# Kernel tuning notes

Hardware: AMD Instinct MI355X
Metric: run time of the kernel (lower is better)

Reference implementation:

```python
import jax, jax.numpy as jnp
import numpy as np
import math

NEG_INF = -1e30  # stand-in for float('-inf'); softmax/logsumexp treat it identically


def _fnoise(x):
    # factorized NoisyNet transform f(x) = sign(x) * sqrt(|x|)
    return jnp.sign(x) * jnp.sqrt(jnp.abs(x))


def setup_inputs() -> dict:
    B, T, D, E = 4, 4096, 2048, 16
    key = jax.random.key(0)
    ks = jax.random.split(key, 6)
    sigma_init = 0.4 / math.sqrt(D)  # sigma_zero / sqrt(in_features)
    return {
        "mh_output": jax.random.normal(ks[0], (B, T, D), dtype=jnp.float32),
        "weight": jax.random.normal(ks[1], (E, D), dtype=jnp.float32) * 0.02,
        "sigma_weight": jnp.full((E, D), sigma_init, dtype=jnp.float32),
        "bias": jax.random.normal(ks[2], (E,), dtype=jnp.float32) * 0.02,
        "sigma_bias": jnp.full((E,), sigma_init, dtype=jnp.float32),
        "eps_in": jax.random.normal(ks[3], (D,), dtype=jnp.float32),
        "eps_out": jax.random.normal(ks[4], (E,), dtype=jnp.float32),
    }


def reference(mh_output, weight, sigma_weight, bias, sigma_bias, eps_in, eps_out):
    top_k = 2
    E = weight.shape[0]

    # NoisyFactorizedLinear: W' = W + sigma_W * (f(eps_out) f(eps_in)^T)
    f_in = _fnoise(eps_in)            # [D]
    f_out = _fnoise(eps_out)          # [E]
    w_noisy = weight + sigma_weight * (f_out[:, None] * f_in[None, :])  # [E, D]
    b_noisy = bias + sigma_bias * f_out                                 # [E]
    logits = jnp.einsum("btd,ed->bte", mh_output, w_noisy) + b_noisy    # [B,T,E]
    # dropout(p=0.125) is identity in eval mode

    top_vals, indices = jax.lax.top_k(logits, top_k)                    # [B,T,k]
    # scatter top-k back into a -inf-filled tensor == mask of selected experts
    keep = jnp.sum(jax.nn.one_hot(indices, E, dtype=jnp.bool_), axis=-2)  # [B,T,E]
    sparse_logits = jnp.where(keep, logits, NEG_INF)

    router_output = jax.nn.softmax(sparse_logits, axis=-1)

    # z-loss: mean(logsumexp(sparse_logits, -1)^2); only top-k entries survive
    lse = jax.scipy.special.logsumexp(top_vals, axis=-1)                # [B,T]
    z_loss = jnp.mean(lse ** 2)

    return router_output, indices, z_loss
```

## Files before the change

kernel.cpp:

```cpp
#include <hip/hip_runtime.h>
#include <math.h>

#define NROWS 16384
#define DDIM  2048
#define NEXP  16
#define RBLOCKS 1024
#define WPB 4
#define ZN (RBLOCKS * WPB)

__device__ __forceinline__ float fnoise(float x) {
    return copysignf(sqrtf(fabsf(x)), x);
}

__device__ __forceinline__ void async_copy16(const float4* g, float4* l) {
    __builtin_amdgcn_global_load_lds(
        (const __attribute__((address_space(1))) void*)g,
        (__attribute__((address_space(3))) void*)l, 16, 0, 0);
}


__global__ void prep_kernel(const float* __restrict__ weight,
                            const float* __restrict__ sigma_weight,
                            const float* __restrict__ bias,
                            const float* __restrict__ sigma_bias,
                            const float* __restrict__ eps_in,
                            const float* __restrict__ eps_out,
                            float* __restrict__ w_noisy,
                            float* __restrict__ b_noisy) {
    int gid = blockIdx.x * blockDim.x + threadIdx.x;
    int e  = gid >> 9;
    int c4 = gid & 511;
    float4 w  = ((const float4*)weight)[gid];
    float4 sw = ((const float4*)sigma_weight)[gid];
    float4 ei = ((const float4*)eps_in)[c4];
    float fo = fnoise(eps_out[e]);
    float4 r;
    r.x = w.x + sw.x * fo * fnoise(ei.x);
    r.y = w.y + sw.y * fo * fnoise(ei.y);
    r.z = w.z + sw.z * fo * fnoise(ei.z);
    r.w = w.w + sw.w * fo * fnoise(ei.w);
    ((float4*)w_noisy)[gid] = r;
    if (gid < 4) {
        float4 b  = ((const float4*)bias)[gid];
        float4 sb = ((const float4*)sigma_bias)[gid];
        float4 eo = ((const float4*)eps_out)[gid];
        float4 rb;
        rb.x = b.x + sb.x * fnoise(eo.x);
        rb.y = b.y + sb.y * fnoise(eo.y);
        rb.z = b.z + sb.z * fnoise(eo.z);
        rb.w = b.w + sb.w * fnoise(eo.w);
        ((float4*)b_noisy)[gid] = rb;
    }
}

__global__ __launch_bounds__(256, 4) void router_kernel(
        const float* __restrict__ x,
        const float* __restrict__ w_noisy,
        const float* __restrict__ b_noisy,
        float* __restrict__ out_router,
        float* __restrict__ out_idx,
        float* __restrict__ zpart) {
    __shared__ float4 wlds[2][NEXP * 64];

    const int tid  = threadIdx.x;
    const int wv   = tid >> 6;
    const int lane = tid & 63;

    const int rowBase = blockIdx.x * 16 + wv * 4;
    const float4* xr0 = (const float4*)(x + (size_t)(rowBase + 0) * DDIM);
    const float4* xr1 = (const float4*)(x + (size_t)(rowBase + 1) * DDIM);
    const float4* xr2 = (const float4*)(x + (size_t)(rowBase + 2) * DDIM);
    const float4* xr3 = (const float4*)(x + (size_t)(rowBase + 3) * DDIM);
    const float4* wsrc = (const float4*)w_noisy;

    float acc[64];
    #pragma unroll
    for (int i = 0; i < 64; ++i) acc[i] = 0.0f;

    float4 xbuf[2][4];

    #pragma unroll
    for (int j = 0; j < 4; ++j) {
        int fb = j * 256 + wv * 64;
        async_copy16(wsrc + (size_t)(fb >> 6) * 512 + lane, &wlds[0][fb]);
    }
    xbuf[0][0] = xr0[lane];
    xbuf[0][1] = xr1[lane];
    xbuf[0][2] = xr2[lane];
    xbuf[0][3] = xr3[lane];
    __syncthreads();

    #pragma unroll
    for (int c = 0; c < 8; ++c) {
        const int cb = c & 1;
        const int nb = cb ^ 1;
        const int xc = c & 1;
        const int xn = xc ^ 1;
        if (c < 7) {
            #pragma unroll
            for (int j = 0; j < 4; ++j) {
                int fb = j * 256 + wv * 64;
                async_copy16(wsrc + (size_t)(fb >> 6) * 512 + (c + 1) * 64 + lane,
                             &wlds[nb][fb]);
            }
            int p = (c + 1) * 64 + lane;
            xbuf[xn][0] = xr0[p];
            xbuf[xn][1] = xr1[p];
            xbuf[xn][2] = xr2[p];
            xbuf[xn][3] = xr3[p];
        }
        #pragma unroll
        for (int e = 0; e < 16; ++e) {
            float4 w = wlds[cb][e * 64 + lane];
            float s0 = acc[0 * 16 + e];
            float s1 = acc[1 * 16 + e];
            float s2 = acc[2 * 16 + e];
            float s3 = acc[3 * 16 + e];
            s0 = fmaf(xbuf[xc][0].x, w.x, s0); s0 = fmaf(xbuf[xc][0].y, w.y, s0);
            s0 = fmaf(xbuf[xc][0].z, w.z, s0); s0 = fmaf(xbuf[xc][0].w, w.w, s0);
            s1 = fmaf(xbuf[xc][1].x, w.x, s1); s1 = fmaf(xbuf[xc][1].y, w.y, s1);
            s1 = fmaf(xbuf[xc][1].z, w.z, s1); s1 = fmaf(xbuf[xc][1].w, w.w, s1);
            s2 = fmaf(xbuf[xc][2].x, w.x, s2); s2 = fmaf(xbuf[xc][2].y, w.y, s2);
            s2 = fmaf(xbuf[xc][2].z, w.z, s2); s2 = fmaf(xbuf[xc][2].w, w.w, s2);
            s3 = fmaf(xbuf[xc][3].x, w.x, s3); s3 = fmaf(xbuf[xc][3].y, w.y, s3);
            s3 = fmaf(xbuf[xc][3].z, w.z, s3); s3 = fmaf(xbuf[xc][3].w, w.w, s3);
            acc[0 * 16 + e] = s0;
            acc[1 * 16 + e] = s1;
            acc[2 * 16 + e] = s2;
            acc[3 * 16 + e] = s3;
        }
        if (c < 7) __syncthreads();
    }

    #pragma unroll
    for (int half = 32; half >= 1; half >>= 1) {
        #pragma unroll
        for (int i = 0; i < half; ++i) {
            bool hi = (lane & half) != 0;
            float keep = hi ? acc[i + half] : acc[i];
            float send = hi ? acc[i] : acc[i + half];
            float recv = __shfl_xor(send, half, 64);
            acc[i] = keep + recv;
        }
    }

    const int e = lane & 15;
    const int r = lane >> 4;
    const int row = rowBase + r;
    float logit = acc[0] + b_noisy[e];

    float m1 = logit; int i1 = e;
    #pragma unroll
    for (int off = 8; off >= 1; off >>= 1) {
        float om = __shfl_xor(m1, off, 64);
        int   oi = __shfl_xor(i1, off, 64);
        if (om > m1 || (om == m1 && oi < i1)) { m1 = om; i1 = oi; }
    }
    float v2 = (e == i1) ? -3.4e38f : logit;
    float m2 = v2; int i2 = e;
    #pragma unroll
    for (int off = 8; off >= 1; off >>= 1) {
        float om = __shfl_xor(m2, off, 64);
        int   oi = __shfl_xor(i2, off, 64);
        if (om > m2 || (om == m2 && oi < i2)) { m2 = om; i2 = oi; }
    }

    float t = expf(m2 - m1);
    float p1 = 1.0f / (1.0f + t);
    float val = (e == i1) ? p1 : ((e == i2) ? t * p1 : 0.0f);
    out_router[(size_t)rowBase * NEXP + lane] = val;

    if (e < 2) {
        out_idx[(size_t)row * 2 + e] = (float)((e == 0) ? i1 : i2);
    }

    float zv = 0.0f;
    if (e == 0) {
        float lse = m1 + log1pf(t);
        zv = lse * lse;
    }
    zv += __shfl_xor(zv, 16, 64);
    zv += __shfl_xor(zv, 32, 64);
    if (lane == 0) {
        zpart[blockIdx.x * WPB + wv] = zv;
    }
}

__global__ void finalize_kernel(const float* __restrict__ zpart,
                                float* __restrict__ out) {
    __shared__ float ws4[4];
    int tid = threadIdx.x;
    float s = 0.0f;
    for (int i = tid; i < ZN; i += 256) s += zpart[i];
    #pragma unroll
    for (int off = 32; off >= 1; off >>= 1) s += __shfl_xor(s, off, 64);
    if ((tid & 63) == 0) ws4[tid >> 6] = s;
    __syncthreads();
    if (tid == 0) {
        float total = ws4[0] + ws4[1] + ws4[2] + ws4[3];
        out[NROWS * NEXP + NROWS * 2] = total * (1.0f / (float)NROWS);
    }
}

extern "C" void kernel_launch(void* const* d_in, const int* in_sizes, int n_in,
                              void* d_out, int out_size, void* d_ws, size_t ws_size,
                              hipStream_t stream) {
    const float* mh      = (const float*)d_in[0];
    const float* weight  = (const float*)d_in[1];
    const float* sigw    = (const float*)d_in[2];
    const float* bias    = (const float*)d_in[3];
    const float* sigb    = (const float*)d_in[4];
    const float* eps_in  = (const float*)d_in[5];
    const float* eps_out = (const float*)d_in[6];

    float* out      = (float*)d_out;
    float* w_noisy  = (float*)d_ws;
    float* b_noisy  = w_noisy + NEXP * DDIM;
    float* zpart    = w_noisy + 32800;

    prep_kernel<<<32, 256, 0, stream>>>(
        weight, sigw, bias, sigb, eps_in, eps_out, w_noisy, b_noisy);

    router_kernel<<<RBLOCKS, 256, 0, stream>>>(
        mh, w_noisy, b_noisy, out, out + NROWS * NEXP, zpart);

    finalize_kernel<<<1, 256, 0, stream>>>(zpart, out);
}
```

Baseline: 211.2 us.

## Fuse noisy weight construction into router kernel, drop prep kernel

Removes the separate prep kernel and builds the noisy weight tile on the fly inside the router kernel. Each block loads weight, sigma and eps_in through registers, applies the factorized noise and writes the result into LDS, replacing the async global-to-LDS copy. The bias noise is also computed inline. This saves one kernel launch and its dependency, but every block now does twice the weight loads plus the noise arithmetic. It also holds more registers across the compute loop, which can hurt occupancy.

```diff
diff --git a/kernel.cpp b/kernel.cpp
--- a/kernel.cpp
+++ b/kernel.cpp
@@ -12,51 +12,15 @@
     return copysignf(sqrtf(fabsf(x)), x);
 }
 
-__device__ __forceinline__ void async_copy16(const float4* g, float4* l) {
-    __builtin_amdgcn_global_load_lds(
-        (const __attribute__((address_space(1))) void*)g,
-        (__attribute__((address_space(3))) void*)l, 16, 0, 0);
-}
-
-
-__global__ void prep_kernel(const float* __restrict__ weight,
-                            const float* __restrict__ sigma_weight,
-                            const float* __restrict__ bias,
-                            const float* __restrict__ sigma_bias,
-                            const float* __restrict__ eps_in,
-                            const float* __restrict__ eps_out,
-                            float* __restrict__ w_noisy,
-                            float* __restrict__ b_noisy) {
-    int gid = blockIdx.x * blockDim.x + threadIdx.x;
-    int e  = gid >> 9;
-    int c4 = gid & 511;
-    float4 w  = ((const float4*)weight)[gid];
-    float4 sw = ((const float4*)sigma_weight)[gid];
-    float4 ei = ((const float4*)eps_in)[c4];
-    float fo = fnoise(eps_out[e]);
-    float4 r;
-    r.x = w.x + sw.x * fo * fnoise(ei.x);
-    r.y = w.y + sw.y * fo * fnoise(ei.y);
-    r.z = w.z + sw.z * fo * fnoise(ei.z);
-    r.w = w.w + sw.w * fo * fnoise(ei.w);
-    ((float4*)w_noisy)[gid] = r;
-    if (gid < 4) {
-        float4 b  = ((const float4*)bias)[gid];
-        float4 sb = ((const float4*)sigma_bias)[gid];
-        float4 eo = ((const float4*)eps_out)[gid];
-        float4 rb;
-        rb.x = b.x + sb.x * fnoise(eo.x);
-        rb.y = b.y + sb.y * fnoise(eo.y);
-        rb.z = b.z + sb.z * fnoise(eo.z);
-        rb.w = b.w + sb.w * fnoise(eo.w);
-        ((float4*)b_noisy)[gid] = rb;
-    }
-}
 
 __global__ __launch_bounds__(256, 4) void router_kernel(
         const float* __restrict__ x,
-        const float* __restrict__ w_noisy,
-        const float* __restrict__ b_noisy,
+        const float* __restrict__ weight,
+        const float* __restrict__ sigma_w,
+        const float* __restrict__ bias,
+        const float* __restrict__ sigma_b,
+        const float* __restrict__ eps_in,
+        const float* __restrict__ eps_out,
         float* __restrict__ out_router,
         float* __restrict__ out_idx,
         float* __restrict__ zpart) {
@@ -71,7 +35,14 @@
     const float4* xr1 = (const float4*)(x + (size_t)(rowBase + 1) * DDIM);
     const float4* xr2 = (const float4*)(x + (size_t)(rowBase + 2) * DDIM);
     const float4* xr3 = (const float4*)(x + (size_t)(rowBase + 3) * DDIM);
-    const float4* wsrc = (const float4*)w_noisy;
+    const float4* wsrc = (const float4*)weight;
+    const float4* ssrc = (const float4*)sigma_w;
+    const float4* eisrc = (const float4*)eps_in;
+
+    float fo0 = fnoise(eps_out[0 * 4 + wv]);
+    float fo1 = fnoise(eps_out[1 * 4 + wv]);
+    float fo2 = fnoise(eps_out[2 * 4 + wv]);
+    float fo3 = fnoise(eps_out[3 * 4 + wv]);
 
     float acc[64];
     #pragma unroll
@@ -79,10 +50,23 @@
 
     float4 xbuf[2][4];
 
-    #pragma unroll
-    for (int j = 0; j < 4; ++j) {
-        int fb = j * 256 + wv * 64;
-        async_copy16(wsrc + (size_t)(fb >> 6) * 512 + lane, &wlds[0][fb]);
+    {
+        float4 ei = eisrc[lane];
+        float fi_x = fnoise(ei.x), fi_y = fnoise(ei.y);
+        float fi_z = fnoise(ei.z), fi_w = fnoise(ei.w);
+        #pragma unroll
+        for (int j = 0; j < 4; ++j) {
+            const float foj = (j == 0) ? fo0 : (j == 1) ? fo1 : (j == 2) ? fo2 : fo3;
+            size_t g = (size_t)(j * 4 + wv) * 512 + lane;
+            float4 w4 = wsrc[g];
+            float4 s4 = ssrc[g];
+            float4 r;
+            r.x = w4.x + s4.x * foj * fi_x;
+            r.y = w4.y + s4.y * foj * fi_y;
+            r.z = w4.z + s4.z * foj * fi_z;
+            r.w = w4.w + s4.w * foj * fi_w;
+            wlds[0][j * 256 + wv * 64 + lane] = r;
+        }
     }
     xbuf[0][0] = xr0[lane];
     xbuf[0][1] = xr1[lane];
@@ -96,13 +80,18 @@
         const int nb = cb ^ 1;
         const int xc = c & 1;
         const int xn = xc ^ 1;
+        float4 w40, w41, w42, w43, s40, s41, s42, s43, ei;
         if (c < 7) {
-            #pragma unroll
-            for (int j = 0; j < 4; ++j) {
-                int fb = j * 256 + wv * 64;
-                async_copy16(wsrc + (size_t)(fb >> 6) * 512 + (c + 1) * 64 + lane,
-                             &wlds[nb][fb]);
-            }
+            size_t col = (size_t)(c + 1) * 64 + lane;
+            ei  = eisrc[col];
+            w40 = wsrc[(size_t)(0 * 4 + wv) * 512 + col];
+            s40 = ssrc[(size_t)(0 * 4 + wv) * 512 + col];
+            w41 = wsrc[(size_t)(1 * 4 + wv) * 512 + col];
+            s41 = ssrc[(size_t)(1 * 4 + wv) * 512 + col];
+            w42 = wsrc[(size_t)(2 * 4 + wv) * 512 + col];
+            s42 = ssrc[(size_t)(2 * 4 + wv) * 512 + col];
+            w43 = wsrc[(size_t)(3 * 4 + wv) * 512 + col];
+            s43 = ssrc[(size_t)(3 * 4 + wv) * 512 + col];
             int p = (c + 1) * 64 + lane;
             xbuf[xn][0] = xr0[p];
             xbuf[xn][1] = xr1[p];
@@ -129,7 +118,24 @@
             acc[2 * 16 + e] = s2;
             acc[3 * 16 + e] = s3;
         }
-        if (c < 7) __syncthreads();
+        if (c < 7) {
+            float fi_x = fnoise(ei.x), fi_y = fnoise(ei.y);
+            float fi_z = fnoise(ei.z), fi_w = fnoise(ei.w);
+            float4 r;
+            r.x = w40.x + s40.x * fo0 * fi_x;  r.y = w40.y + s40.y * fo0 * fi_y;
+            r.z = w40.z + s40.z * fo0 * fi_z;  r.w = w40.w + s40.w * fo0 * fi_w;
+            wlds[nb][0 * 256 + wv * 64 + lane] = r;
+            r.x = w41.x + s41.x * fo1 * fi_x;  r.y = w41.y + s41.y * fo1 * fi_y;
+            r.z = w41.z + s41.z * fo1 * fi_z;  r.w = w41.w + s41.w * fo1 * fi_w;
+            wlds[nb][1 * 256 + wv * 64 + lane] = r;
+            r.x = w42.x + s42.x * fo2 * fi_x;  r.y = w42.y + s42.y * fo2 * fi_y;
+            r.z = w42.z + s42.z * fo2 * fi_z;  r.w = w42.w + s42.w * fo2 * fi_w;
+            wlds[nb][2 * 256 + wv * 64 + lane] = r;
+            r.x = w43.x + s43.x * fo3 * fi_x;  r.y = w43.y + s43.y * fo3 * fi_y;
+            r.z = w43.z + s43.z * fo3 * fi_z;  r.w = w43.w + s43.w * fo3 * fi_w;
+            wlds[nb][3 * 256 + wv * 64 + lane] = r;
+            __syncthreads();
+        }
     }
 
     #pragma unroll
@@ -147,7 +153,7 @@
     const int e = lane & 15;
     const int r = lane >> 4;
     const int row = rowBase + r;
-    float logit = acc[0] + b_noisy[e];
+    float logit = acc[0] + (bias[e] + sigma_b[e] * fnoise(eps_out[e]));
 
     float m1 = logit; int i1 = e;
     #pragma unroll
@@ -213,16 +219,12 @@
     const float* eps_in  = (const float*)d_in[5];
     const float* eps_out = (const float*)d_in[6];
 
-    float* out      = (float*)d_out;
-    float* w_noisy  = (float*)d_ws;
-    float* b_noisy  = w_noisy + NEXP * DDIM;
-    float* zpart    = w_noisy + 32800;
-
-    prep_kernel<<<32, 256, 0, stream>>>(
-        weight, sigw, bias, sigb, eps_in, eps_out, w_noisy, b_noisy);
+    float* out   = (float*)d_out;
+    float* zpart = (float*)d_ws + 32800;
 
     router_kernel<<<RBLOCKS, 256, 0, stream>>>(
-        mh, w_noisy, b_noisy, out, out + NROWS * NEXP, zpart);
+        mh, weight, sigw, bias, sigb, eps_in, eps_out,
+        out, out + NROWS * NEXP, zpart);
 
     finalize_kernel<<<1, 256, 0, stream>>>(zpart, out);
 }
```

Measured after the change: 218.9 us. 3.7% more time.

## Use 8 waves per block with 2 rows per wave to cut register pressure

Applied to the files above, without the earlier changes.

The router block goes from 256 to 512 threads. Each wave now handles 2 rows instead of 4, which halves the accumulator and x-buffer registers so more waves can be resident. The butterfly reduction gains an extra xor-32 shuffle, and only the lower half of each wave writes outputs. In exchange, each weight value read from LDS is reused across fewer rows, which doubles LDS reads per FMA.

```diff
diff --git a/kernel.cpp b/kernel.cpp
--- a/kernel.cpp
+++ b/kernel.cpp
@@ -5,7 +5,7 @@
 #define DDIM  2048
 #define NEXP  16
 #define RBLOCKS 1024
-#define WPB 4
+#define WPB 8
 #define ZN (RBLOCKS * WPB)
 
 __device__ __forceinline__ float fnoise(float x) {
@@ -53,7 +53,7 @@
     }
 }
 
-__global__ __launch_bounds__(256, 4) void router_kernel(
+__global__ __launch_bounds__(512, 6) void router_kernel(
         const float* __restrict__ x,
         const float* __restrict__ w_noisy,
         const float* __restrict__ b_noisy,
@@ -66,28 +66,24 @@
     const int wv   = tid >> 6;
     const int lane = tid & 63;
 
-    const int rowBase = blockIdx.x * 16 + wv * 4;
+    const int rowBase = blockIdx.x * 16 + wv * 2;
     const float4* xr0 = (const float4*)(x + (size_t)(rowBase + 0) * DDIM);
     const float4* xr1 = (const float4*)(x + (size_t)(rowBase + 1) * DDIM);
-    const float4* xr2 = (const float4*)(x + (size_t)(rowBase + 2) * DDIM);
-    const float4* xr3 = (const float4*)(x + (size_t)(rowBase + 3) * DDIM);
     const float4* wsrc = (const float4*)w_noisy;
 
-    float acc[64];
-    #pragma unroll
-    for (int i = 0; i < 64; ++i) acc[i] = 0.0f;
-
-    float4 xbuf[2][4];
-
-    #pragma unroll
-    for (int j = 0; j < 4; ++j) {
-        int fb = j * 256 + wv * 64;
+    float acc[32];
+    #pragma unroll
+    for (int i = 0; i < 32; ++i) acc[i] = 0.0f;
+
+    float4 xbuf[2][2];
+
+    #pragma unroll
+    for (int j = 0; j < 2; ++j) {
+        int fb = j * 512 + wv * 64;
         async_copy16(wsrc + (size_t)(fb >> 6) * 512 + lane, &wlds[0][fb]);
     }
     xbuf[0][0] = xr0[lane];
     xbuf[0][1] = xr1[lane];
-    xbuf[0][2] = xr2[lane];
-    xbuf[0][3] = xr3[lane];
     __syncthreads();
 
     #pragma unroll
@@ -98,42 +94,34 @@
         const int xn = xc ^ 1;
         if (c < 7) {
             #pragma unroll
-            for (int j = 0; j < 4; ++j) {
-                int fb = j * 256 + wv * 64;
+            for (int j = 0; j < 2; ++j) {
+                int fb = j * 512 + wv * 64;
                 async_copy16(wsrc + (size_t)(fb >> 6) * 512 + (c + 1) * 64 + lane,
                              &wlds[nb][fb]);
             }
             int p = (c + 1) * 64 + lane;
             xbuf[xn][0] = xr0[p];
             xbuf[xn][1] = xr1[p];
-            xbuf[xn][2] = xr2[p];
-            xbuf[xn][3] = xr3[p];
         }
         #pragma unroll
         for (int e = 0; e < 16; ++e) {
             float4 w = wlds[cb][e * 64 + lane];
-            float s0 = acc[0 * 16 + e];
-            float s1 = acc[1 * 16 + e];
-            float s2 = acc[2 * 16 + e];
-            float s3 = acc[3 * 16 + e];
+            float s0 = acc[e];
+            float s1 = acc[16 + e];
             s0 = fmaf(xbuf[xc][0].x, w.x, s0); s0 = fmaf(xbuf[xc][0].y, w.y, s0);
             s0 = fmaf(xbuf[xc][0].z, w.z, s0); s0 = fmaf(xbuf[xc][0].w, w.w, s0);
             s1 = fmaf(xbuf[xc][1].x, w.x, s1); s1 = fmaf(xbuf[xc][1].y, w.y, s1);
             s1 = fmaf(xbuf[xc][1].z, w.z, s1); s1 = fmaf(xbuf[xc][1].w, w.w, s1);
-            s2 = fmaf(xbuf[xc][2].x, w.x, s2); s2 = fmaf(xbuf[xc][2].y, w.y, s2);
-            s2 = fmaf(xbuf[xc][2].z, w.z, s2); s2 = fmaf(xbuf[xc][2].w, w.w, s2);
-            s3 = fmaf(xbuf[xc][3].x, w.x, s3); s3 = fmaf(xbuf[xc][3].y, w.y, s3);
-            s3 = fmaf(xbuf[xc][3].z, w.z, s3); s3 = fmaf(xbuf[xc][3].w, w.w, s3);
-            acc[0 * 16 + e] = s0;
-            acc[1 * 16 + e] = s1;
-            acc[2 * 16 + e] = s2;
-            acc[3 * 16 + e] = s3;
+            acc[e]      = s0;
+            acc[16 + e] = s1;
         }
         if (c < 7) __syncthreads();
     }
 
     #pragma unroll
-    for (int half = 32; half >= 1; half >>= 1) {
+    for (int i = 0; i < 32; ++i) acc[i] += __shfl_xor(acc[i], 32, 64);
+    #pragma unroll
+    for (int half = 16; half >= 1; half >>= 1) {
         #pragma unroll
         for (int i = 0; i < half; ++i) {
             bool hi = (lane & half) != 0;
@@ -145,7 +133,7 @@
     }
 
     const int e = lane & 15;
-    const int r = lane >> 4;
+    const int r = (lane >> 4) & 1;
     const int row = rowBase + r;
     float logit = acc[0] + b_noisy[e];
 
@@ -168,14 +156,15 @@
     float t = expf(m2 - m1);
     float p1 = 1.0f / (1.0f + t);
     float val = (e == i1) ? p1 : ((e == i2) ? t * p1 : 0.0f);
-    out_router[(size_t)rowBase * NEXP + lane] = val;
-
-    if (e < 2) {
-        out_idx[(size_t)row * 2 + e] = (float)((e == 0) ? i1 : i2);
+    if (lane < 32) {
+        out_router[(size_t)rowBase * NEXP + lane] = val;
+        if (e < 2) {
+            out_idx[(size_t)row * 2 + e] = (float)((e == 0) ? i1 : i2);
+        }
     }
 
     float zv = 0.0f;
-    if (e == 0) {
+    if (e == 0 && lane < 32) {
         float lse = m1 + log1pf(t);
         zv = lse * lse;
     }
@@ -221,7 +210,7 @@
     prep_kernel<<<32, 256, 0, stream>>>(
         weight, sigw, bias, sigb, eps_in, eps_out, w_noisy, b_noisy);
 
-    router_kernel<<<RBLOCKS, 256, 0, stream>>>(
+    router_kernel<<<RBLOCKS, 512, 0, stream>>>(
         mh, w_noisy, b_noisy, out, out + NROWS * NEXP, zpart);
 
     finalize_kernel<<<1, 256, 0, stream>>>(zpart, out);
```

Result: slower. 218.4 us (+3.4%).
